# Performance work log

Measured on AMD Instinct MI355X. Metric: run time of the kernel, lower is better.

## Reference

```python
import jax, jax.numpy as jnp
import numpy as np

DIM = 384
NUM_HEADS = 12
WS = 8            # window_size
SS = 4            # shift_size
HEAD_DIM = DIM // NUM_HEADS
SCALE = HEAD_DIM ** -0.5
N = WS * WS       # tokens per window
EPS = 1e-5
MLP_HIDDEN = 4 * DIM

# relative position index (static, matches torch buffer construction)
_coords = np.stack(np.meshgrid(np.arange(WS), np.arange(WS), indexing='ij')).reshape(2, -1)
_rel = (_coords[:, :, None] - _coords[:, None, :]).transpose(1, 2, 0)  # [N,N,2]
_rel[..., 0] += WS - 1
_rel[..., 1] += WS - 1
_rel[..., 0] *= 2 * WS - 1
RPI = jnp.asarray(_rel.sum(-1))  # [N,N] int


def layer_norm(x, g, b):
    m = x.mean(-1, keepdims=True)
    v = ((x - m) ** 2).mean(-1, keepdims=True)
    return (x - m) / jnp.sqrt(v + EPS) * g + b


def window_partition(x):
    B, Hh, Ww, C = x.shape
    x = x.reshape(B, Hh // WS, WS, Ww // WS, WS, C).transpose(0, 1, 3, 2, 4, 5)
    return x.reshape(-1, WS, WS, C)


def window_reverse(w, Hh, Ww):
    B = w.shape[0] // ((Hh // WS) * (Ww // WS))
    x = w.reshape(B, Hh // WS, Ww // WS, WS, WS, -1).transpose(0, 1, 3, 2, 4, 5)
    return x.reshape(B, Hh, Ww, -1)


def attention_mask(Hp, Wp):
    # region id along each axis: 0 = [0, Hp-WS), 1 = [Hp-WS, Hp-SS), 2 = [Hp-SS, Hp)
    h_id = np.zeros(Hp, np.int32); h_id[Hp - WS:Hp - SS] = 1; h_id[Hp - SS:] = 2
    w_id = np.zeros(Wp, np.int32); w_id[Wp - WS:Wp - SS] = 1; w_id[Wp - SS:] = 2
    cnt = h_id[:, None] * 3 + w_id[None, :]                      # [Hp, Wp]
    img = jnp.asarray(cnt, jnp.float32).reshape(1, Hp, Wp, 1)
    mw = window_partition(img).reshape(-1, N)                    # [nW, N]
    am = mw[:, None, :] - mw[:, :, None]                         # [nW, N, N]
    return jnp.where(am != 0, jnp.float32(-100.0), jnp.float32(0.0))


def setup_inputs() -> dict:
    key = jax.random.key(0)
    ks = jax.random.split(key, 8)
    B, H, W = 32, 64, 64
    std = 0.02
    return {
        'x': jax.random.normal(ks[0], (B, H * W, DIM), jnp.float32),
        'qkv_w': jax.random.normal(ks[1], (DIM, 3 * DIM), jnp.float32) * std,
        'qkv_b': jnp.zeros((3 * DIM,), jnp.float32),
        'proj_w': jax.random.normal(ks[2], (DIM, DIM), jnp.float32) * std,
        'proj_b': jnp.zeros((DIM,), jnp.float32),
        'rpb_table': jax.random.normal(ks[3], ((2 * WS - 1) * (2 * WS - 1), NUM_HEADS), jnp.float32) * std,
        'n1_g': jnp.ones((DIM,), jnp.float32), 'n1_b': jnp.zeros((DIM,), jnp.float32),
        'n2_g': jnp.ones((DIM,), jnp.float32), 'n2_b': jnp.zeros((DIM,), jnp.float32),
        'fc1_w': jax.random.normal(ks[4], (DIM, MLP_HIDDEN), jnp.float32) * std,
        'fc1_b': jnp.zeros((MLP_HIDDEN,), jnp.float32),
        'fc2_w': jax.random.normal(ks[5], (MLP_HIDDEN, DIM), jnp.float32) * std,
        'fc2_b': jnp.zeros((DIM,), jnp.float32),
        'H': 64, 'W': 64,
    }


def reference(x, qkv_w, qkv_b, proj_w, proj_b, rpb_table, n1_g, n1_b, n2_g, n2_b,
              fc1_w, fc1_b, fc2_w, fc2_b, H, W):
    B, L, C = x.shape
    shortcut = x
    h = layer_norm(x, n1_g, n1_b).reshape(B, H, W, C)
    pad_r = (WS - W % WS) % WS
    pad_b = (WS - H % WS) % WS
    if pad_r or pad_b:
        h = jnp.pad(h, ((0, 0), (0, pad_b), (0, pad_r), (0, 0)))
    Hp, Wp = H + pad_b, W + pad_r
    shifted = jnp.roll(h, shift=(-SS, -SS), axis=(1, 2))
    xw = window_partition(shifted).reshape(-1, N, C)             # [B_, N, C]
    B_ = xw.shape[0]

    qkv = (xw @ qkv_w + qkv_b).reshape(B_, N, 3, NUM_HEADS, HEAD_DIM)
    q = qkv[:, :, 0].transpose(0, 2, 1, 3) * SCALE               # [B_, h, N, d]
    k = qkv[:, :, 1].transpose(0, 2, 1, 3)
    v = qkv[:, :, 2].transpose(0, 2, 1, 3)

    attn = jnp.einsum('bhnd,bhmd->bhnm', q, k)                   # [B_, h, N, N]
    bias = rpb_table[RPI].transpose(2, 0, 1)                     # [h, N, N]
    attn = attn + bias[None]

    mask = attention_mask(Hp, Wp)                                # [nW, N, N]
    nW = mask.shape[0]
    attn = attn.reshape(B_ // nW, nW, NUM_HEADS, N, N) + mask[None, :, None]
    attn = jax.nn.softmax(attn.reshape(B_, NUM_HEADS, N, N), axis=-1)

    out = jnp.einsum('bhnm,bhmd->bhnd', attn, v)
    out = out.transpose(0, 2, 1, 3).reshape(B_, N, C)
    out = out @ proj_w + proj_b

    out = window_reverse(out.reshape(-1, WS, WS, C), Hp, Wp)
    out = jnp.roll(out, shift=(SS, SS), axis=(1, 2))
    out = out[:, :H, :W, :].reshape(B, H * W, C)

    x = shortcut + out
    h2 = layer_norm(x, n2_g, n2_b)
    mlp = jax.nn.gelu(h2 @ fc1_w + fc1_b, approximate=False) @ fc2_w + fc2_b
    return x + mlp
```

## Files before the change

kernel.cpp:

```cpp
#include <hip/hip_runtime.h>
#include <math.h>


#define ROWS_TOTAL 131072
#define NWIN_TOTAL 2048

typedef __attribute__((ext_vector_type(8))) __bf16 bf16x8;
typedef __attribute__((ext_vector_type(4))) float f32x4;
typedef __attribute__((ext_vector_type(8))) unsigned short ushort8;

__device__ __forceinline__ unsigned short f2bf(float f) {
  unsigned u = __builtin_bit_cast(unsigned, f);
  u = (u + 0x7fffu + ((u >> 16) & 1u)) >> 16;
  return (unsigned short)u;
}
__device__ __forceinline__ float bf2f(unsigned short u) {
  return __builtin_bit_cast(float, (unsigned)u << 16);
}

__device__ __forceinline__ void gload16(const void* g, void* l) {
  __builtin_amdgcn_global_load_lds(
      (const __attribute__((address_space(1))) unsigned int*)g,
      (__attribute__((address_space(3))) unsigned int*)l, 16, 0, 0);
}

__device__ __forceinline__ int gather_row(int win, int t) {
  int b = win >> 6, wi = (win >> 3) & 7, wj = win & 7;
  int gi = (wi * 8 + (t >> 3) + 4) & 63;
  int gj = (wj * 8 + (t & 7) + 4) & 63;
  return (b << 12) + (gi << 6) + gj;
}

__device__ __forceinline__ float gelu_f(float v) {
  float x = v * 0.70710678118654752f;
  float ax = fabsf(x);
  float t = 1.f / (1.f + 0.3275911f * ax);
  float poly =
      t * (0.254829592f +
           t * (-0.284496736f +
                t * (1.421413741f + t * (-1.453152027f + t * 1.061405429f))));
  float er = 1.f - poly * __expf(-x * x);
  er = copysignf(er, x);
  return 0.5f * v * (1.f + er);
}

#define VM4() asm volatile("s_waitcnt vmcnt(4)" ::: "memory")
#define VM0() asm volatile("s_waitcnt vmcnt(0)" ::: "memory")
#define ABAR() asm volatile("s_barrier" ::: "memory")

#define STGA_(buf_, kt_, c_)                                          \
  gload16(aSrcC[c_] + (size_t)(kt_) * 64,                             \
          (char*)As + (buf_) * 32768 + (c_) * 8192 + w * 1024)
#define STGB_(buf_, kt_, c_)                                          \
  gload16(bSrcC[c_] + (size_t)(kt_) * 64,                             \
          (char*)Bs + (buf_) * 24576 + (c_) * 8192 + w * 1024)

#define GEMM_DECLS()                                                  \
  f32x4 acc[8][3];                                                    \
  _Pragma("unroll") for (int i_ = 0; i_ < 8; ++i_)                    \
  _Pragma("unroll") for (int j_ = 0; j_ < 3; ++j_)                    \
      acc[i_][j_] = (f32x4)(0.f);                                     \
  const int sl0 = ((hi) ^ (lr & 7)) * 8;                              \
  const int sl1 = ((4 + hi) ^ (lr & 7)) * 8;                          \
  const int aB0 = (wr * 128 + lr) * 64 + sl0;                         \
  const int aB1 = (wr * 128 + lr) * 64 + sl1;                         \
  const int bB0 = (wc * 48 + lr) * 64 + sl0;                          \
  const int bB1 = (wc * 48 + lr) * 64 + sl1;

#define GEMM_CORE(NT_)                                                \
  {                                                                   \
    STGA_(0, 0, 0); STGA_(0, 0, 1); STGA_(0, 0, 2); STGA_(0, 0, 3);   \
    STGB_(0, 0, 0); STGB_(0, 0, 1); STGB_(0, 0, 2);                   \
    STGA_(1, 1, 0); STGA_(1, 1, 1); STGA_(1, 1, 2); STGA_(1, 1, 3);   \
    VM4(); ABAR();                                                    \
    int curA = 0;                                                     \
    for (int t = 0; t < (NT_); ++t) {                                 \
      const int curB = t & 1;                                         \
      const ushort* AsC = (const ushort*)As + curA * 16384;           \
      const ushort* BsC = (const ushort*)Bs + curB * 12288;           \
      if (t + 1 < (NT_)) {                                            \
        STGB_(curB ^ 1, t + 1, 0);                                    \
        STGB_(curB ^ 1, t + 1, 1);                                    \
        STGB_(curB ^ 1, t + 1, 2);                                    \
      }                                                               \
      if (t + 2 < (NT_)) {                                            \
        int nbA = curA + 2; if (nbA >= 3) nbA -= 3;                   \
        STGA_(nbA, t + 2, 0); STGA_(nbA, t + 2, 1);                   \
        STGA_(nbA, t + 2, 2); STGA_(nbA, t + 2, 3);                   \
      }                                                               \
      bf16x8 bv0[3], bv1[3];                                          \
      _Pragma("unroll") for (int nj = 0; nj < 3; ++nj) {              \
        bv0[nj] = *(const bf16x8*)(BsC + bB0 + nj * 1024);            \
        bv1[nj] = *(const bf16x8*)(BsC + bB1 + nj * 1024);            \
      }                                                               \
      _Pragma("unroll") for (int mi = 0; mi < 8; ++mi) {              \
        bf16x8 a0 = *(const bf16x8*)(AsC + aB0 + mi * 1024);          \
        bf16x8 a1 = *(const bf16x8*)(AsC + aB1 + mi * 1024);          \
        _Pragma("unroll") for (int nj = 0; nj < 3; ++nj) {            \
          acc[mi][nj] = __builtin_amdgcn_mfma_f32_16x16x32_bf16(      \
              a0, bv0[nj], acc[mi][nj], 0, 0, 0);                     \
          acc[mi][nj] = __builtin_amdgcn_mfma_f32_16x16x32_bf16(      \
              a1, bv1[nj], acc[mi][nj], 0, 0, 0);                     \
        }                                                             \
      }                                                               \
      if (t + 2 < (NT_)) { VM4(); ABAR(); }                           \
      else if (t + 1 < (NT_)) { VM0(); ABAR(); }                      \
      ++curA; if (curA == 3) curA = 0;                                \
    }                                                                 \
  }

#define GRID_SWZ(NP_)                                                 \
  int p, bm;                                                          \
  {                                                                   \
    int lin = blockIdx.y * (NP_) + blockIdx.x;                        \
    if ((gridDim.y & 7) == 0) {                                       \
      int xcd = lin & 7, q = lin >> 3;                                \
      p = q % (NP_); bm = (q / (NP_)) * 8 + xcd;                      \
    } else { p = blockIdx.x; bm = blockIdx.y; }                       \
  }

__global__ __launch_bounds__(256) void wprep_k(
    const float* __restrict__ qkvw, const float* __restrict__ projw,
    const float* __restrict__ fc1w, const float* __restrict__ fc2w,
    ushort* __restrict__ wq, ushort* __restrict__ wp,
    ushort* __restrict__ w1, ushort* __restrict__ w2) {
  int gid = blockIdx.x * 256 + threadIdx.x;
  const int S1 = 1152 * 384;
  const int S2 = S1 + 384 * 384;
  const int S3 = S2 + 1536 * 384;
  const int S4 = S3 + 384 * 1536;
  if (gid < S1) {
    int n = gid / 384, k = gid - n * 384;
    wq[gid] = f2bf(qkvw[(size_t)k * 1152 + n]);
  } else if (gid < S2) {
    int i = gid - S1, n = i / 384, k = i - n * 384;
    wp[i] = f2bf(projw[(size_t)k * 384 + n]);
  } else if (gid < S3) {
    int i = gid - S2, n = i / 384, k = i - n * 384;
    w1[i] = f2bf(fc1w[(size_t)k * 1536 + n]);
  } else if (gid < S4) {
    int i = gid - S3, n = i / 1536, k = i - n * 1536;
    w2[i] = f2bf(fc2w[(size_t)k * 384 + n]);
  }
}

__global__ __launch_bounds__(256) void ln_fused_k(
    const float* __restrict__ x, const float* __restrict__ g,
    const float* __restrict__ b, ushort* __restrict__ o) {
  int wid = threadIdx.x >> 6, lane = threadIdx.x & 63;
  int row = (blockIdx.x << 2) + wid;
  const float* p = x + (size_t)row * 384;
  float2 v[3];
  float s = 0.f, ss = 0.f;
#pragma unroll
  for (int c = 0; c < 3; ++c) {
    v[c] = *(const float2*)(p + lane * 2 + c * 128);
    s += v[c].x + v[c].y;
    ss += v[c].x * v[c].x + v[c].y * v[c].y;
  }
#pragma unroll
  for (int off = 1; off < 64; off <<= 1) {
    s += __shfl_xor(s, off);
    ss += __shfl_xor(ss, off);
  }
  float m = s * (1.f / 384.f);
  float r = rsqrtf(ss * (1.f / 384.f) - m * m + 1e-5f);
  ushort* op = o + (size_t)row * 384;
#pragma unroll
  for (int c = 0; c < 3; ++c) {
    float2 gg = *(const float2*)(g + lane * 2 + c * 128);
    float2 bb = *(const float2*)(b + lane * 2 + c * 128);
    union { ushort u[2]; unsigned w; } pk;
    pk.u[0] = f2bf((v[c].x - m) * r * gg.x + bb.x);
    pk.u[1] = f2bf((v[c].y - m) * r * gg.y + bb.y);
    *(unsigned*)(op + lane * 2 + c * 128) = pk.w;
  }
}

__global__ __launch_bounds__(512, 2) void qkv_mfma_k(
    const ushort* __restrict__ xln, const ushort* __restrict__ wq,
    const float* __restrict__ qkvb, ushort* __restrict__ qkvd, int wc0) {
  __shared__ __align__(16) ushort As[3][16384];
  __shared__ __align__(16) ushort Bs[2][12288];
  const int tid = threadIdx.x;
  const int w = tid >> 6, lane = tid & 63;
  const int wr = w >> 2, wc = w & 3;
  const int lr = lane & 15, hi = lane >> 4;
  GRID_SWZ(6);
  const int n0 = p * 192;
  const int sg = ((tid & 7) ^ ((tid >> 3) & 7)) * 8;
  const ushort* aSrcC[4];
  const ushort* bSrcC[3];
#pragma unroll
  for (int c = 0; c < 4; ++c)
    aSrcC[c] =
        xln + (size_t)gather_row(wc0 + bm * 4 + c, tid >> 3) * 384 + sg;
#pragma unroll
  for (int c = 0; c < 3; ++c)
    bSrcC[c] = wq + (size_t)(n0 + c * 64 + (tid >> 3)) * 384 + sg;
  GEMM_DECLS();
  GEMM_CORE(6);
  const float scale = 0.17677669529663687f;
#pragma unroll
  for (int mi = 0; mi < 8; ++mi) {
#pragma unroll
    for (int r = 0; r < 4; ++r) {
      int rr = wr * 128 + mi * 16 + (hi << 2) + r;
      size_t row = (size_t)(bm * 256 + rr);
#pragma unroll
      for (int nj = 0; nj < 3; ++nj) {
        int nc = n0 + wc * 48 + nj * 16 + lr;
        float v = acc[mi][nj][r] + qkvb[nc];
        if (nc < 384) v *= scale;
        qkvd[row * 1152 + nc] = f2bf(v);
      }
    }
  }
}

__global__ __launch_bounds__(128) void attn_k(
    const ushort* __restrict__ qkv, const float* __restrict__ rpb,
    ushort* __restrict__ ao, int wc0) {
  __shared__ __align__(16) float kbuf[2][64][32];
  __shared__ __align__(16) float vbuf[2][64][32];
  __shared__ float bias[2][232];
  __shared__ int region[64];
  const int tid = threadIdx.x;
  const int wid = tid >> 6, lane = tid & 63;
  const int w = blockIdx.x, win = wc0 + w;
  const int head = blockIdx.y * 2 + wid;
  if (tid < 64) {
    int wi = (win >> 3) & 7, wj = win & 7;
    int pi = wi * 8 + (tid >> 3), pj = wj * 8 + (tid & 7);
    int ri = pi < 56 ? 0 : (pi < 60 ? 1 : 2);
    int rj = pj < 56 ? 0 : (pj < 60 ? 1 : 2);
    region[tid] = ri * 3 + rj;
  }
  const ushort* base = qkv + (size_t)(w * 64) * 1152;
  const int kcol = 384 + head * 32, vcol = 768 + head * 32;
#pragma unroll
  for (int s = 0; s < 4; ++s) {
    int f = s * 64 + lane;
    int r = f >> 2, c = (f & 3) * 8;
    ushort8 ku = *(const ushort8*)(base + (size_t)r * 1152 + kcol + c);
    ushort8 vu = *(const ushort8*)(base + (size_t)r * 1152 + vcol + c);
#pragma unroll
    for (int j = 0; j < 8; ++j) {
      kbuf[wid][r][c + j] = bf2f(ku[j]);
      vbuf[wid][r][c + j] = bf2f(vu[j]);
    }
  }
  for (int s = lane; s < 225; s += 64) bias[wid][s] = rpb[s * 12 + head];
  __syncthreads();
  const int i = lane;
  float qr[32];
  const ushort* qp = base + (size_t)i * 1152 + head * 32;
#pragma unroll
  for (int c = 0; c < 4; ++c) {
    ushort8 qu = *(const ushort8*)(qp + c * 8);
#pragma unroll
    for (int j = 0; j < 8; ++j) qr[c * 8 + j] = bf2f(qu[j]);
  }
  const int yi = i >> 3, xi = i & 7, regi = region[i];
  float sc[64];
  float mx = -3.0e38f;
#pragma unroll
  for (int j = 0; j < 64; ++j) {
    float a = 0.f;
#pragma unroll
    for (int c = 0; c < 32; c += 4) {
      float4 kv = *(float4*)&kbuf[wid][j][c];
      a = fmaf(qr[c], kv.x, a);
      a = fmaf(qr[c + 1], kv.y, a);
      a = fmaf(qr[c + 2], kv.z, a);
      a = fmaf(qr[c + 3], kv.w, a);
    }
    int dy = yi - (j >> 3) + 7, dx = xi - (j & 7) + 7;
    a += bias[wid][dy * 15 + dx];
    if (region[j] != regi) a -= 100.f;
    sc[j] = a;
    mx = fmaxf(mx, a);
  }
  float sum = 0.f;
#pragma unroll
  for (int j = 0; j < 64; ++j) {
    float e = __expf(sc[j] - mx);
    sc[j] = e;
    sum += e;
  }
  const float inv = 1.f / sum;
  float o[32];
#pragma unroll
  for (int c = 0; c < 32; ++c) o[c] = 0.f;
#pragma unroll
  for (int j = 0; j < 64; ++j) {
    float p = sc[j];
#pragma unroll
    for (int c = 0; c < 32; c += 4) {
      float4 vv = *(float4*)&vbuf[wid][j][c];
      o[c] = fmaf(p, vv.x, o[c]);
      o[c + 1] = fmaf(p, vv.y, o[c + 1]);
      o[c + 2] = fmaf(p, vv.z, o[c + 2]);
      o[c + 3] = fmaf(p, vv.w, o[c + 3]);
    }
  }
  ushort* op = ao + ((size_t)(w * 64 + i)) * 384 + (head << 5);
#pragma unroll
  for (int c = 0; c < 32; c += 8) {
    ushort8 pk;
#pragma unroll
    for (int j2 = 0; j2 < 8; ++j2) pk[j2] = f2bf(o[c + j2] * inv);
    *(ushort8*)(op + c) = pk;
  }
}

__global__ __launch_bounds__(512, 2) void proj_mfma_k(
    const ushort* __restrict__ ao, const ushort* __restrict__ wp,
    const float* __restrict__ pb, const float* __restrict__ x,
    float* __restrict__ x2, int wc0) {
  __shared__ __align__(16) ushort As[3][16384];
  __shared__ __align__(16) ushort Bs[2][12288];
  const int tid = threadIdx.x;
  const int w = tid >> 6, lane = tid & 63;
  const int wr = w >> 2, wc = w & 3;
  const int lr = lane & 15, hi = lane >> 4;
  GRID_SWZ(2);
  const int n0 = p * 192;
  const int sg = ((tid & 7) ^ ((tid >> 3) & 7)) * 8;
  const ushort* aSrcC[4];
  const ushort* bSrcC[3];
#pragma unroll
  for (int c = 0; c < 4; ++c)
    aSrcC[c] = ao + (size_t)(bm * 256 + c * 64 + (tid >> 3)) * 384 + sg;
#pragma unroll
  for (int c = 0; c < 3; ++c)
    bSrcC[c] = wp + (size_t)(n0 + c * 64 + (tid >> 3)) * 384 + sg;
  GEMM_DECLS();
  GEMM_CORE(6);
#pragma unroll
  for (int mi = 0; mi < 8; ++mi) {
#pragma unroll
    for (int r = 0; r < 4; ++r) {
      int rr = wr * 128 + mi * 16 + (hi << 2) + r;
      int gl = bm * 256 + rr;
      int gr = gather_row(wc0 + (gl >> 6), gl & 63);
#pragma unroll
      for (int nj = 0; nj < 3; ++nj) {
        int nc = n0 + wc * 48 + nj * 16 + lr;
        size_t idx = (size_t)gr * 384 + nc;
        x2[idx] = acc[mi][nj][r] + pb[nc] + x[idx];
      }
    }
  }
}

__global__ __launch_bounds__(512, 2) void fc1_mfma_k(
    const ushort* __restrict__ x2ln, const ushort* __restrict__ w1,
    const float* __restrict__ fb, ushort* __restrict__ hm, int row0) {
  __shared__ __align__(16) ushort As[3][16384];
  __shared__ __align__(16) ushort Bs[2][12288];
  const int tid = threadIdx.x;
  const int w = tid >> 6, lane = tid & 63;
  const int wr = w >> 2, wc = w & 3;
  const int lr = lane & 15, hi = lane >> 4;
  GRID_SWZ(8);
  const int n0 = p * 192;
  const int sg = ((tid & 7) ^ ((tid >> 3) & 7)) * 8;
  const ushort* aSrcC[4];
  const ushort* bSrcC[3];
#pragma unroll
  for (int c = 0; c < 4; ++c)
    aSrcC[c] =
        x2ln + (size_t)(row0 + bm * 256 + c * 64 + (tid >> 3)) * 384 + sg;
#pragma unroll
  for (int c = 0; c < 3; ++c)
    bSrcC[c] = w1 + (size_t)(n0 + c * 64 + (tid >> 3)) * 384 + sg;
  GEMM_DECLS();
  GEMM_CORE(6);
#pragma unroll
  for (int mi = 0; mi < 8; ++mi) {
#pragma unroll
    for (int r = 0; r < 4; ++r) {
      int rr = wr * 128 + mi * 16 + (hi << 2) + r;
      size_t lrow = (size_t)(bm * 256 + rr);
#pragma unroll
      for (int nj = 0; nj < 3; ++nj) {
        int nc = n0 + wc * 48 + nj * 16 + lr;
        float v = gelu_f(acc[mi][nj][r] + fb[nc]);
        hm[lrow * 1536 + nc] = f2bf(v);
      }
    }
  }
}

__global__ __launch_bounds__(512, 2) void fc2_mfma_k(
    const ushort* __restrict__ hm, const ushort* __restrict__ w2,
    const float* __restrict__ fb, float* __restrict__ out, int row0) {
  __shared__ __align__(16) ushort As[3][16384];
  __shared__ __align__(16) ushort Bs[2][12288];
  const int tid = threadIdx.x;
  const int w = tid >> 6, lane = tid & 63;
  const int wr = w >> 2, wc = w & 3;
  const int lr = lane & 15, hi = lane >> 4;
  GRID_SWZ(2);
  const int n0 = p * 192;
  const int sg = ((tid & 7) ^ ((tid >> 3) & 7)) * 8;
  const ushort* aSrcC[4];
  const ushort* bSrcC[3];
#pragma unroll
  for (int c = 0; c < 4; ++c)
    aSrcC[c] = hm + (size_t)(bm * 256 + c * 64 + (tid >> 3)) * 1536 + sg;
#pragma unroll
  for (int c = 0; c < 3; ++c)
    bSrcC[c] = w2 + (size_t)(n0 + c * 64 + (tid >> 3)) * 1536 + sg;
  GEMM_DECLS();
  GEMM_CORE(24);
#pragma unroll
  for (int mi = 0; mi < 8; ++mi) {
#pragma unroll
    for (int r = 0; r < 4; ++r) {
      int rr = wr * 128 + mi * 16 + (hi << 2) + r;
      size_t grow = (size_t)(row0 + bm * 256 + rr);
#pragma unroll
      for (int nj = 0; nj < 3; ++nj) {
        int nc = n0 + wc * 48 + nj * 16 + lr;
        size_t idx = grow * 384 + nc;
        out[idx] = out[idx] + acc[mi][nj][r] + fb[nc];
      }
    }
  }
}

extern "C" void kernel_launch(void* const* d_in, const int* in_sizes, int n_in,
                              void* d_out, int out_size, void* d_ws, size_t ws_size,
                              hipStream_t stream) {
  const float* x = (const float*)d_in[0];
  const float* qkv_w = (const float*)d_in[1];
  const float* qkv_b = (const float*)d_in[2];
  const float* proj_w = (const float*)d_in[3];
  const float* proj_b = (const float*)d_in[4];
  const float* rpb = (const float*)d_in[5];
  const float* n1g = (const float*)d_in[6];
  const float* n1b = (const float*)d_in[7];
  const float* n2g = (const float*)d_in[8];
  const float* n2b = (const float*)d_in[9];
  const float* fc1w = (const float*)d_in[10];
  const float* fc1b = (const float*)d_in[11];
  const float* fc2w = (const float*)d_in[12];
  const float* fc2b = (const float*)d_in[13];
  float* out = (float*)d_out;
  char* ws = (char*)d_ws;

  ushort* wq = (ushort*)ws;
  ushort* wp = wq + 442368;
  ushort* w1 = wp + 147456;
  ushort* w2 = w1 + 589824;
  ushort* xln = (ushort*)(ws + 3538944);
  char* scratch = ws + 3538944 + 100663296;
  size_t base = 3538944 + 100663296;
  size_t ssz = (ws_size > base) ? ws_size - base : 0;

  wprep_k<<<6912, 256, 0, stream>>>(qkv_w, proj_w, fc1w, fc2w, wq, wp, w1, w2);
  ln_fused_k<<<ROWS_TOTAL / 4, 256, 0, stream>>>(x, n1g, n1b, xln);

  const size_t perwin = 196608;
  int nwc = (int)(ssz / perwin);
  if (nwc > NWIN_TOTAL) nwc = NWIN_TOTAL;
  nwc &= ~31;
  if (nwc < 32) nwc = 32;
  ushort* qkvd = (ushort*)scratch;
  ushort* ao = qkvd + (size_t)nwc * 73728;
  for (int wc0 = 0; wc0 < NWIN_TOTAL; wc0 += nwc) {
    int nw = (NWIN_TOTAL - wc0 < nwc) ? (NWIN_TOTAL - wc0) : nwc;
    qkv_mfma_k<<<dim3(6, nw / 4), 512, 0, stream>>>(xln, wq, qkv_b, qkvd, wc0);
    attn_k<<<dim3(nw, 6), 128, 0, stream>>>(qkvd, rpb, ao, wc0);
    proj_mfma_k<<<dim3(2, nw / 4), 512, 0, stream>>>(ao, wp, proj_b, x, out,
                                                     wc0);
  }

  ln_fused_k<<<ROWS_TOTAL / 4, 256, 0, stream>>>(out, n2g, n2b, xln);
  const size_t pergrp = 786432;
  int ngc = (int)(ssz / pergrp);
  if (ngc > 512) ngc = 512;
  ngc &= ~7;
  if (ngc < 8) ngc = 8;
  ushort* hm = (ushort*)scratch;
  for (int g0 = 0; g0 < 512; g0 += ngc) {
    int ng = (512 - g0 < ngc) ? (512 - g0) : ngc;
    fc1_mfma_k<<<dim3(8, ng), 512, 0, stream>>>(xln, w1, fc1b, hm, g0 * 256);
    fc2_mfma_k<<<dim3(2, ng), 512, 0, stream>>>(hm, w2, fc2b, out, g0 * 256);
  }
}
```

Baseline: 1.549 ms.

## Shrink GEMM tiles to 128x96 with 256-thread blocks and simple double buffering

Replaces the 256x192, 512-thread GEMM core with a 128x96, 256-thread core for all four projection/MLP GEMMs. The K-step drops from 64 to 32 and the three-stage swizzled pipeline becomes a plain double buffer synchronised with __syncthreads. The goal is more blocks, smaller LDS use and higher occupancy. In exchange, each tile gets less operand reuse, barriers run more often, and the LDS layout is no longer swizzled, which may cause bank conflicts.

```diff
diff --git a/kernel.cpp b/kernel.cpp
--- a/kernel.cpp
+++ b/kernel.cpp
@@ -44,79 +44,58 @@
   return 0.5f * v * (1.f + er);
 }
 
-#define VM4() asm volatile("s_waitcnt vmcnt(4)" ::: "memory")
-#define VM0() asm volatile("s_waitcnt vmcnt(0)" ::: "memory")
-#define ABAR() asm volatile("s_barrier" ::: "memory")
-
-#define STGA_(buf_, kt_, c_)                                          \
-  gload16(aSrcC[c_] + (size_t)(kt_) * 64,                             \
-          (char*)As + (buf_) * 32768 + (c_) * 8192 + w * 1024)
-#define STGB_(buf_, kt_, c_)                                          \
-  gload16(bSrcC[c_] + (size_t)(kt_) * 64,                             \
-          (char*)Bs + (buf_) * 24576 + (c_) * 8192 + w * 1024)
-
-#define GEMM_DECLS()                                                  \
-  f32x4 acc[8][3];                                                    \
-  _Pragma("unroll") for (int i_ = 0; i_ < 8; ++i_)                    \
-  _Pragma("unroll") for (int j_ = 0; j_ < 3; ++j_)                    \
-      acc[i_][j_] = (f32x4)(0.f);                                     \
-  const int sl0 = ((hi) ^ (lr & 7)) * 8;                              \
-  const int sl1 = ((4 + hi) ^ (lr & 7)) * 8;                          \
-  const int aB0 = (wr * 128 + lr) * 64 + sl0;                         \
-  const int aB1 = (wr * 128 + lr) * 64 + sl1;                         \
-  const int bB0 = (wc * 48 + lr) * 64 + sl0;                          \
-  const int bB1 = (wc * 48 + lr) * 64 + sl1;
-
-#define GEMM_CORE(NT_)                                                \
-  {                                                                   \
-    STGA_(0, 0, 0); STGA_(0, 0, 1); STGA_(0, 0, 2); STGA_(0, 0, 3);   \
-    STGB_(0, 0, 0); STGB_(0, 0, 1); STGB_(0, 0, 2);                   \
-    STGA_(1, 1, 0); STGA_(1, 1, 1); STGA_(1, 1, 2); STGA_(1, 1, 3);   \
-    VM4(); ABAR();                                                    \
-    int curA = 0;                                                     \
-    for (int t = 0; t < (NT_); ++t) {                                 \
-      const int curB = t & 1;                                         \
-      const ushort* AsC = (const ushort*)As + curA * 16384;           \
-      const ushort* BsC = (const ushort*)Bs + curB * 12288;           \
-      if (t + 1 < (NT_)) {                                            \
-        STGB_(curB ^ 1, t + 1, 0);                                    \
-        STGB_(curB ^ 1, t + 1, 1);                                    \
-        STGB_(curB ^ 1, t + 1, 2);                                    \
-      }                                                               \
-      if (t + 2 < (NT_)) {                                            \
-        int nbA = curA + 2; if (nbA >= 3) nbA -= 3;                   \
-        STGA_(nbA, t + 2, 0); STGA_(nbA, t + 2, 1);                   \
-        STGA_(nbA, t + 2, 2); STGA_(nbA, t + 2, 3);                   \
-      }                                                               \
-      bf16x8 bv0[3], bv1[3];                                          \
-      _Pragma("unroll") for (int nj = 0; nj < 3; ++nj) {              \
-        bv0[nj] = *(const bf16x8*)(BsC + bB0 + nj * 1024);            \
-        bv1[nj] = *(const bf16x8*)(BsC + bB1 + nj * 1024);            \
-      }                                                               \
-      _Pragma("unroll") for (int mi = 0; mi < 8; ++mi) {              \
-        bf16x8 a0 = *(const bf16x8*)(AsC + aB0 + mi * 1024);          \
-        bf16x8 a1 = *(const bf16x8*)(AsC + aB1 + mi * 1024);          \
-        _Pragma("unroll") for (int nj = 0; nj < 3; ++nj) {            \
-          acc[mi][nj] = __builtin_amdgcn_mfma_f32_16x16x32_bf16(      \
-              a0, bv0[nj], acc[mi][nj], 0, 0, 0);                     \
-          acc[mi][nj] = __builtin_amdgcn_mfma_f32_16x16x32_bf16(      \
-              a1, bv1[nj], acc[mi][nj], 0, 0, 0);                     \
-        }                                                             \
-      }                                                               \
-      if (t + 2 < (NT_)) { VM4(); ABAR(); }                           \
-      else if (t + 1 < (NT_)) { VM0(); ABAR(); }                      \
-      ++curA; if (curA == 3) curA = 0;                                \
-    }                                                                 \
-  }
-
-#define GRID_SWZ(NP_)                                                 \
-  int p, bm;                                                          \
-  {                                                                   \
-    int lin = blockIdx.y * (NP_) + blockIdx.x;                        \
-    if ((gridDim.y & 7) == 0) {                                       \
-      int xcd = lin & 7, q = lin >> 3;                                \
-      p = q % (NP_); bm = (q / (NP_)) * 8 + xcd;                      \
-    } else { p = blockIdx.x; bm = blockIdx.y; }                       \
+#define STG(buf_, t_)                                                   \
+  {                                                                     \
+    size_t ko = (size_t)(t_) * 64;                                      \
+    gload16(aS0 + ko, (char*)As + (buf_) * 8192 + tid * 16);            \
+    gload16(aS1 + ko, (char*)As + (buf_) * 8192 + 4096 + tid * 16);     \
+    gload16(bS0 + ko, (char*)Bs + (buf_) * 6144 + tid * 16);            \
+    if (tid < 128)                                                      \
+      gload16(bS1 + ko, (char*)Bs + (buf_) * 6144 + 4096 + tid * 16);   \
+  }
+
+#define GEMM_DECLS()                                                    \
+  f32x4 acc[4][3];                                                      \
+  _Pragma("unroll") for (int i_ = 0; i_ < 4; ++i_)                      \
+  _Pragma("unroll") for (int j_ = 0; j_ < 3; ++j_)                      \
+      acc[i_][j_] = (f32x4)(0.f);                                       \
+  int aO[4], bO[3];                                                     \
+  _Pragma("unroll") for (int mi_ = 0; mi_ < 4; ++mi_)                   \
+      aO[mi_] = (wr * 64 + mi_ * 16 + lr) * 32 + hi * 8;                \
+  _Pragma("unroll") for (int nj_ = 0; nj_ < 3; ++nj_)                   \
+      bO[nj_] = (wc * 48 + nj_ * 16 + lr) * 32 + hi * 8;
+
+#define GEMM_CORE(NT_)                                                  \
+  {                                                                     \
+    int cur = 0;                                                        \
+    STG(0, 0);                                                          \
+    __syncthreads();                                                    \
+    for (int t = 0; t < (NT_); ++t) {                                   \
+      if (t + 1 < (NT_)) STG(cur ^ 1, t + 1);                           \
+      const ushort* AsC = &As[cur][0];                                  \
+      const ushort* BsC = &Bs[cur][0];                                  \
+      bf16x8 bv[3];                                                     \
+      _Pragma("unroll") for (int nj = 0; nj < 3; ++nj)                  \
+          bv[nj] = *(const bf16x8*)(BsC + bO[nj]);                      \
+      _Pragma("unroll") for (int mi = 0; mi < 4; ++mi) {                \
+        bf16x8 av = *(const bf16x8*)(AsC + aO[mi]);                     \
+        _Pragma("unroll") for (int nj = 0; nj < 3; ++nj)                \
+          acc[mi][nj] = __builtin_amdgcn_mfma_f32_16x16x32_bf16(        \
+              av, bv[nj], acc[mi][nj], 0, 0, 0);                        \
+      }                                                                 \
+      __syncthreads();                                                  \
+      cur ^= 1;                                                         \
+    }                                                                   \
+  }
+
+#define GRID_SWZ(NP_)                                                   \
+  int p, bm;                                                            \
+  {                                                                     \
+    int lin = blockIdx.y * (NP_) + blockIdx.x;                          \
+    if ((gridDim.y & 7) == 0) {                                         \
+      int xcd = lin & 7, q = lin >> 3;                                  \
+      p = q % (NP_); bm = (q / (NP_)) * 8 + xcd;                        \
+    } else { p = blockIdx.x; bm = blockIdx.y; }                         \
   }
 
 __global__ __launch_bounds__(256) void wprep_k(
@@ -177,36 +156,38 @@
   }
 }
 
-__global__ __launch_bounds__(512, 2) void qkv_mfma_k(
+__global__ __launch_bounds__(256) void qkv_mfma_k(
     const ushort* __restrict__ xln, const ushort* __restrict__ wq,
     const float* __restrict__ qkvb, ushort* __restrict__ qkvd, int wc0) {
-  __shared__ __align__(16) ushort As[3][16384];
-  __shared__ __align__(16) ushort Bs[2][12288];
+  __shared__ __align__(16) ushort As[2][4096];
+  __shared__ __align__(16) ushort Bs[2][3072];
   const int tid = threadIdx.x;
-  const int w = tid >> 6, lane = tid & 63;
-  const int wr = w >> 2, wc = w & 3;
+  const int lane = tid & 63;
+  const int w = tid >> 6;
+  const int wr = w >> 1, wc = w & 1;
   const int lr = lane & 15, hi = lane >> 4;
-  GRID_SWZ(6);
-  const int n0 = p * 192;
-  const int sg = ((tid & 7) ^ ((tid >> 3) & 7)) * 8;
-  const ushort* aSrcC[4];
-  const ushort* bSrcC[3];
-#pragma unroll
-  for (int c = 0; c < 4; ++c)
-    aSrcC[c] =
-        xln + (size_t)gather_row(wc0 + bm * 4 + c, tid >> 3) * 384 + sg;
-#pragma unroll
-  for (int c = 0; c < 3; ++c)
-    bSrcC[c] = wq + (size_t)(n0 + c * 64 + (tid >> 3)) * 384 + sg;
+  GRID_SWZ(12);
+  const int n0 = p * 96;
+  int r0 = tid >> 2, r1 = (256 + tid) >> 2;
+  const char* aS0 = (const char*)xln +
+                    (size_t)gather_row(wc0 + bm * 2 + (r0 >> 6), r0 & 63) * 768 +
+                    (tid & 3) * 16;
+  const char* aS1 = (const char*)xln +
+                    (size_t)gather_row(wc0 + bm * 2 + (r1 >> 6), r1 & 63) * 768 +
+                    ((256 + tid) & 3) * 16;
+  const char* bS0 = (const char*)wq + (size_t)(n0 + (tid >> 2)) * 768 +
+                    (tid & 3) * 16;
+  const char* bS1 = (const char*)wq + (size_t)(n0 + 64 + (tid >> 2)) * 768 +
+                    (tid & 3) * 16;
   GEMM_DECLS();
-  GEMM_CORE(6);
+  GEMM_CORE(12);
   const float scale = 0.17677669529663687f;
 #pragma unroll
-  for (int mi = 0; mi < 8; ++mi) {
+  for (int mi = 0; mi < 4; ++mi) {
 #pragma unroll
     for (int r = 0; r < 4; ++r) {
-      int rr = wr * 128 + mi * 16 + (hi << 2) + r;
-      size_t row = (size_t)(bm * 256 + rr);
+      int rr = wr * 64 + mi * 16 + (hi << 2) + r;
+      size_t row = (size_t)(bm * 128 + rr);
 #pragma unroll
       for (int nj = 0; nj < 3; ++nj) {
         int nc = n0 + wc * 48 + nj * 16 + lr;
@@ -314,35 +295,35 @@
   }
 }
 
-__global__ __launch_bounds__(512, 2) void proj_mfma_k(
+__global__ __launch_bounds__(256) void proj_mfma_k(
     const ushort* __restrict__ ao, const ushort* __restrict__ wp,
     const float* __restrict__ pb, const float* __restrict__ x,
     float* __restrict__ x2, int wc0) {
-  __shared__ __align__(16) ushort As[3][16384];
-  __shared__ __align__(16) ushort Bs[2][12288];
+  __shared__ __align__(16) ushort As[2][4096];
+  __shared__ __align__(16) ushort Bs[2][3072];
   const int tid = threadIdx.x;
-  const int w = tid >> 6, lane = tid & 63;
-  const int wr = w >> 2, wc = w & 3;
+  const int lane = tid & 63;
+  const int w = tid >> 6;
+  const int wr = w >> 1, wc = w & 1;
   const int lr = lane & 15, hi = lane >> 4;
-  GRID_SWZ(2);
-  const int n0 = p * 192;
-  const int sg = ((tid & 7) ^ ((tid >> 3) & 7)) * 8;
-  const ushort* aSrcC[4];
-  const ushort* bSrcC[3];
-#pragma unroll
-  for (int c = 0; c < 4; ++c)
-    aSrcC[c] = ao + (size_t)(bm * 256 + c * 64 + (tid >> 3)) * 384 + sg;
-#pragma unroll
-  for (int c = 0; c < 3; ++c)
-    bSrcC[c] = wp + (size_t)(n0 + c * 64 + (tid >> 3)) * 384 + sg;
+  GRID_SWZ(4);
+  const int n0 = p * 96;
+  const char* aS0 = (const char*)ao +
+                    (size_t)(bm * 128 + (tid >> 2)) * 768 + (tid & 3) * 16;
+  const char* aS1 = (const char*)ao +
+                    (size_t)(bm * 128 + 64 + (tid >> 2)) * 768 + (tid & 3) * 16;
+  const char* bS0 = (const char*)wp + (size_t)(n0 + (tid >> 2)) * 768 +
+                    (tid & 3) * 16;
+  const char* bS1 = (const char*)wp + (size_t)(n0 + 64 + (tid >> 2)) * 768 +
+                    (tid & 3) * 16;
   GEMM_DECLS();
-  GEMM_CORE(6);
-#pragma unroll
-  for (int mi = 0; mi < 8; ++mi) {
+  GEMM_CORE(12);
+#pragma unroll
+  for (int mi = 0; mi < 4; ++mi) {
 #pragma unroll
     for (int r = 0; r < 4; ++r) {
-      int rr = wr * 128 + mi * 16 + (hi << 2) + r;
-      int gl = bm * 256 + rr;
+      int rr = wr * 64 + mi * 16 + (hi << 2) + r;
+      int gl = bm * 128 + rr;
       int gr = gather_row(wc0 + (gl >> 6), gl & 63);
 #pragma unroll
       for (int nj = 0; nj < 3; ++nj) {
@@ -354,35 +335,36 @@
   }
 }
 
-__global__ __launch_bounds__(512, 2) void fc1_mfma_k(
+__global__ __launch_bounds__(256) void fc1_mfma_k(
     const ushort* __restrict__ x2ln, const ushort* __restrict__ w1,
     const float* __restrict__ fb, ushort* __restrict__ hm, int row0) {
-  __shared__ __align__(16) ushort As[3][16384];
-  __shared__ __align__(16) ushort Bs[2][12288];
+  __shared__ __align__(16) ushort As[2][4096];
+  __shared__ __align__(16) ushort Bs[2][3072];
   const int tid = threadIdx.x;
-  const int w = tid >> 6, lane = tid & 63;
-  const int wr = w >> 2, wc = w & 3;
+  const int lane = tid & 63;
+  const int w = tid >> 6;
+  const int wr = w >> 1, wc = w & 1;
   const int lr = lane & 15, hi = lane >> 4;
-  GRID_SWZ(8);
-  const int n0 = p * 192;
-  const int sg = ((tid & 7) ^ ((tid >> 3) & 7)) * 8;
-  const ushort* aSrcC[4];
-  const ushort* bSrcC[3];
-#pragma unroll
-  for (int c = 0; c < 4; ++c)
-    aSrcC[c] =
-        x2ln + (size_t)(row0 + bm * 256 + c * 64 + (tid >> 3)) * 384 + sg;
-#pragma unroll
-  for (int c = 0; c < 3; ++c)
-    bSrcC[c] = w1 + (size_t)(n0 + c * 64 + (tid >> 3)) * 384 + sg;
+  GRID_SWZ(16);
+  const int n0 = p * 96;
+  const char* aS0 = (const char*)x2ln +
+                    (size_t)(row0 + bm * 128 + (tid >> 2)) * 768 +
+                    (tid & 3) * 16;
+  const char* aS1 = (const char*)x2ln +
+                    (size_t)(row0 + bm * 128 + 64 + (tid >> 2)) * 768 +
+                    (tid & 3) * 16;
+  const char* bS0 = (const char*)w1 + (size_t)(n0 + (tid >> 2)) * 768 +
+                    (tid & 3) * 16;
+  const char* bS1 = (const char*)w1 + (size_t)(n0 + 64 + (tid >> 2)) * 768 +
+                    (tid & 3) * 16;
   GEMM_DECLS();
-  GEMM_CORE(6);
-#pragma unroll
-  for (int mi = 0; mi < 8; ++mi) {
+  GEMM_CORE(12);
+#pragma unroll
+  for (int mi = 0; mi < 4; ++mi) {
 #pragma unroll
     for (int r = 0; r < 4; ++r) {
-      int rr = wr * 128 + mi * 16 + (hi << 2) + r;
-      size_t lrow = (size_t)(bm * 256 + rr);
+      int rr = wr * 64 + mi * 16 + (hi << 2) + r;
+      size_t lrow = (size_t)(bm * 128 + rr);
 #pragma unroll
       for (int nj = 0; nj < 3; ++nj) {
         int nc = n0 + wc * 48 + nj * 16 + lr;
@@ -393,34 +375,35 @@
   }
 }
 
-__global__ __launch_bounds__(512, 2) void fc2_mfma_k(
+__global__ __launch_bounds__(256) void fc2_mfma_k(
     const ushort* __restrict__ hm, const ushort* __restrict__ w2,
     const float* __restrict__ fb, float* __restrict__ out, int row0) {
-  __shared__ __align__(16) ushort As[3][16384];
-  __shared__ __align__(16) ushort Bs[2][12288];
+  __shared__ __align__(16) ushort As[2][4096];
+  __shared__ __align__(16) ushort Bs[2][3072];
   const int tid = threadIdx.x;
-  const int w = tid >> 6, lane = tid & 63;
-  const int wr = w >> 2, wc = w & 3;
+  const int lane = tid & 63;
+  const int w = tid >> 6;
+  const int wr = w >> 1, wc = w & 1;
   const int lr = lane & 15, hi = lane >> 4;
-  GRID_SWZ(2);
-  const int n0 = p * 192;
-  const int sg = ((tid & 7) ^ ((tid >> 3) & 7)) * 8;
-  const ushort* aSrcC[4];
-  const ushort* bSrcC[3];
-#pragma unroll
-  for (int c = 0; c < 4; ++c)
-    aSrcC[c] = hm + (size_t)(bm * 256 + c * 64 + (tid >> 3)) * 1536 + sg;
-#pragma unroll
-  for (int c = 0; c < 3; ++c)
-    bSrcC[c] = w2 + (size_t)(n0 + c * 64 + (tid >> 3)) * 1536 + sg;
+  GRID_SWZ(4);
+  const int n0 = p * 96;
+  const char* aS0 = (const char*)hm +
+                    (size_t)(bm * 128 + (tid >> 2)) * 3072 + (tid & 3) * 16;
+  const char* aS1 = (const char*)hm +
+                    (size_t)(bm * 128 + 64 + (tid >> 2)) * 3072 +
+                    (tid & 3) * 16;
+  const char* bS0 = (const char*)w2 + (size_t)(n0 + (tid >> 2)) * 3072 +
+                    (tid & 3) * 16;
+  const char* bS1 = (const char*)w2 + (size_t)(n0 + 64 + (tid >> 2)) * 3072 +
+                    (tid & 3) * 16;
   GEMM_DECLS();
-  GEMM_CORE(24);
-#pragma unroll
-  for (int mi = 0; mi < 8; ++mi) {
+  GEMM_CORE(48);
+#pragma unroll
+  for (int mi = 0; mi < 4; ++mi) {
 #pragma unroll
     for (int r = 0; r < 4; ++r) {
-      int rr = wr * 128 + mi * 16 + (hi << 2) + r;
-      size_t grow = (size_t)(row0 + bm * 256 + rr);
+      int rr = wr * 64 + mi * 16 + (hi << 2) + r;
+      size_t grow = (size_t)(row0 + bm * 128 + rr);
 #pragma unroll
       for (int nj = 0; nj < 3; ++nj) {
         int nc = n0 + wc * 48 + nj * 16 + lr;
@@ -472,22 +455,23 @@
   ushort* ao = qkvd + (size_t)nwc * 73728;
   for (int wc0 = 0; wc0 < NWIN_TOTAL; wc0 += nwc) {
     int nw = (NWIN_TOTAL - wc0 < nwc) ? (NWIN_TOTAL - wc0) : nwc;
-    qkv_mfma_k<<<dim3(6, nw / 4), 512, 0, stream>>>(xln, wq, qkv_b, qkvd, wc0);
+    qkv_mfma_k<<<dim3(12, nw / 2), 256, 0, stream>>>(xln, wq, qkv_b, qkvd,
+                                                     wc0);
     attn_k<<<dim3(nw, 6), 128, 0, stream>>>(qkvd, rpb, ao, wc0);
-    proj_mfma_k<<<dim3(2, nw / 4), 512, 0, stream>>>(ao, wp, proj_b, x, out,
+    proj_mfma_k<<<dim3(4, nw / 2), 256, 0, stream>>>(ao, wp, proj_b, x, out,
                                                      wc0);
   }
 
   ln_fused_k<<<ROWS_TOTAL / 4, 256, 0, stream>>>(out, n2g, n2b, xln);
-  const size_t pergrp = 786432;
+  const size_t pergrp = 393216;
   int ngc = (int)(ssz / pergrp);
-  if (ngc > 512) ngc = 512;
+  if (ngc > 1024) ngc = 1024;
   ngc &= ~7;
   if (ngc < 8) ngc = 8;
   ushort* hm = (ushort*)scratch;
-  for (int g0 = 0; g0 < 512; g0 += ngc) {
-    int ng = (512 - g0 < ngc) ? (512 - g0) : ngc;
-    fc1_mfma_k<<<dim3(8, ng), 512, 0, stream>>>(xln, w1, fc1b, hm, g0 * 256);
-    fc2_mfma_k<<<dim3(2, ng), 512, 0, stream>>>(hm, w2, fc2b, out, g0 * 256);
-  }
-}
+  for (int g0 = 0; g0 < 1024; g0 += ngc) {
+    int ng = (1024 - g0 < ngc) ? (1024 - g0) : ngc;
+    fc1_mfma_k<<<dim3(16, ng), 256, 0, stream>>>(xln, w1, fc1b, hm, g0 * 128);
+    fc2_mfma_k<<<dim3(4, ng), 256, 0, stream>>>(hm, w2, fc2b, out, g0 * 128);
+  }
+}
```

Result: no change. 1.548 ms (-0.0%).
